# Performance work log

Measured on AMD Instinct MI355X. Metric: run time of the kernel, lower is better.

The kernel has to match this reference:

```python
import jax, jax.numpy as jnp
import numpy as np

NX, NY = 256, 256            # img_size
NUM_DET, VIEW = 368, 180
SDD, SCD = 1000.0, 500.0
DCD = SDD - SCD
DET_INT = 2.0
PX = 1.0                     # pixel_size
SHIFT = 0.0                  # no quarter offset


def _geometry():
    # Faithful numpy port of FP.param_setting (equally_spaced mode)
    d_beta = np.pi * 360.0 / VIEW / 180.0
    beta = np.linspace(0.0, (VIEW - 1) * d_beta, VIEW)
    axis_x = np.linspace(-NX / 2, NX / 2, NX + 1) * PX          # [NX+1]
    axis_y = np.linspace(-NY / 2, NY / 2, NY + 1) * PX          # [NY+1]
    range_det_x = np.ones(NUM_DET) * DCD
    range_det_y = np.linspace(-(NUM_DET - 1) / 2, (NUM_DET - 1) / 2, NUM_DET) * DET_INT + SHIFT
    src = np.array([-SCD, 0.0])
    cb, sb = np.cos(beta), np.sin(beta)
    src_point = np.stack([src[0] * cb + src[1] * sb, -src[0] * sb + src[1] * cb])  # [2, V]
    det_x_rot = cb[None, :] * range_det_x[:, None] + sb[None, :] * range_det_y[:, None]   # [D, V]
    det_y_rot = -sb[None, :] * range_det_x[:, None] + cb[None, :] * range_det_y[:, None]  # [D, V]
    ax = (axis_x[:, None] - src_point[0][None, :])[None, :, :] / (det_x_rot - src_point[0])[:, None, :]  # [D, NX+1, V]
    ay = (axis_y[:, None] - src_point[1][None, :])[None, :, :] / (det_y_rot - src_point[1])[:, None, :]  # [D, NY+1, V]
    a_min = np.maximum(np.minimum(ax[:, 0, :], ax[:, -1, :]), np.minimum(ay[:, 0, :], ay[:, -1, :]))
    a_min[a_min < 0] = 0.0
    a_max = np.minimum(np.maximum(ax[:, 0, :], ax[:, -1, :]), np.maximum(ay[:, 0, :], ay[:, -1, :]))
    a_max[a_max > 1] = 1.0
    axy = np.concatenate([ax, ay], axis=1)                       # [D, NX+NY+2, V]
    axy[(axy > a_max[:, None, :]) | (axy < a_min[:, None, :])] = np.nan
    axy = np.sort(axy, axis=1)                                   # NaNs sort to the end (matches torch)
    diff_axy = np.diff(axy, n=1, axis=1)                         # [D, S, V], S = NX+NY+1
    a_mid = axy[:, :-1, :] + diff_axy / 2
    diff_axy = np.nan_to_num(diff_axy, nan=0.0)
    a_mid = np.nan_to_num(a_mid, nan=0.0)
    s2d = np.sqrt((det_x_rot - src_point[0]) ** 2 + (det_y_rot - src_point[1]) ** 2)  # [D, V]
    weighting = diff_axy.transpose(0, 2, 1)[None, None] * s2d[None, None, :, :, None]  # [1,1,D,V,S]
    x_pos = a_mid * (det_x_rot[:, None, :] - src_point[0]) + src_point[0]
    x_pos = x_pos.transpose(0, 2, 1) / (PX * (NX - 1) / 2)       # [D, V, S]
    y_pos = a_mid * (det_y_rot[:, None, :] - src_point[1]) + src_point[1]
    y_pos = y_pos.transpose(0, 2, 1) / (PX * (NY - 1) / 2)
    grid_pos = np.stack([x_pos, y_pos], axis=-1)                 # [D, V, S, 2]
    return grid_pos.astype(np.float32), weighting.astype(np.float32)


def _bilinear_sample(img, gx, gy):
    # torch.nn.functional.grid_sample: bilinear, padding_mode='zeros', align_corners=False
    # img: [B,C,H,W]; gx indexes W, gy indexes H; gx/gy: [D,V,S]
    B, C, H, W = img.shape
    ix = ((gx + 1.0) * W - 1.0) * 0.5
    iy = ((gy + 1.0) * H - 1.0) * 0.5
    ix0 = jnp.floor(ix)
    iy0 = jnp.floor(iy)
    wx1 = ix - ix0
    wy1 = iy - iy0
    out = jnp.zeros((B, C) + gx.shape, dtype=img.dtype)
    for dx in (0, 1):
        for dy in (0, 1):
            xi = ix0 + dx
            yi = iy0 + dy
            w = (wx1 if dx else 1.0 - wx1) * (wy1 if dy else 1.0 - wy1)
            valid = (xi >= 0) & (xi < W) & (yi >= 0) & (yi < H)
            xi_c = jnp.clip(xi, 0, W - 1).astype(jnp.int32)
            yi_c = jnp.clip(yi, 0, H - 1).astype(jnp.int32)
            out = out + img[:, :, yi_c, xi_c] * (w * valid)[None, None]
    return out  # [B,C,D,V,S]


def setup_inputs() -> dict:
    key = jax.random.key(0)
    img = jax.random.normal(key, (1, 1, NX, NY), dtype=jnp.float32)
    gp, wt = _geometry()
    return {"img": img, "grid_pos": jnp.asarray(gp), "weighting": jnp.asarray(wt)}


def reference(img, grid_pos, weighting):
    # All views vectorized at once (torch version loops over views)
    interp = _bilinear_sample(img, grid_pos[..., 0], grid_pos[..., 1])  # [B,C,D,V,S]
    sino = jnp.sum(weighting * interp, axis=-1)                         # [B,C,D,V]
    return jnp.where(jnp.isnan(sino), jnp.zeros((), sino.dtype), sino)
```

## Files before the change

kernel.cpp:

```cpp
#include <hip/hip_runtime.h>
#include <hip/hip_fp16.h>
#include <math.h>


constexpr int IMG_N  = 256;
constexpr int NDET   = 368;
constexpr int NVIEW  = 180;
constexpr int NSAMP  = 2 * IMG_N + 1;
constexpr int DV     = NDET * NVIEW;
constexpr int NITER  = (NSAMP + 63) / 64;

struct __align__(8) Corner { __half2 ab; __half2 cd; };

constexpr size_t PACK_BYTES = (size_t)IMG_N * IMG_N * sizeof(Corner);
constexpr size_t RT_OFF     = PACK_BYTES;
constexpr size_t RT_BYTES   = (size_t)DV * 3 * sizeof(float4);
constexpr size_t KR_OFF     = RT_OFF + RT_BYTES;
constexpr size_t KR_BYTES   = (size_t)DV * sizeof(int2);
constexpr size_t WS_NEEDED  = KR_OFF + KR_BYTES;

__device__ __forceinline__ double valAP(double A, double s, double inv, int k) {
    return (A + s * (double)k) * inv;
}

__global__ __launch_bounds__(256) void pack_kernel(
    const float* __restrict__ img, Corner* __restrict__ P)
{
    const int idx = blockIdx.x * 256 + threadIdx.x;
    const int y  = idx >> 8;
    const int x  = idx & 255;
    const int x1 = min(x + 1, IMG_N - 1);
    const int y1 = min(y + 1, IMG_N - 1);
    Corner c;
    c.ab = __floats2half2_rn(img[y * IMG_N + x],  img[y * IMG_N + x1]);
    c.cd = __floats2half2_rn(img[y1 * IMG_N + x], img[y1 * IMG_N + x1]);
    P[idx] = c;
}

__global__ __launch_bounds__(256) void geom_kernel(
    float4* __restrict__ rt, int2* __restrict__ kr)
{
    const int idx = blockIdx.x * 256 + threadIdx.x;
    if (idx >= DV) return;
    const int d = idx / NVIEW;
    const int v = idx - d * NVIEW;

    const double d_beta = ((M_PI * 360.0) / (double)NVIEW) / 180.0;
    const double stop   = (double)(NVIEW - 1) * d_beta;
    const double step   = stop / (double)(NVIEW - 1);
    const double beta   = (v == NVIEW - 1) ? stop : (double)v * step;
    const double cb = cos(beta), sb = sin(beta);

    const double sx  = -500.0 * cb;
    const double sy  =  500.0 * sb;
    const double rdy = ((double)d - 183.5) * 2.0;
    const double dx  = cb * 500.0 + sb * rdy;
    const double dy  = (-sb) * 500.0 + cb * rdy;
    const double ddx = dx - sx, ddy = dy - sy;

    double Ax, sxn;
    const double invx = 1.0 / ddx;
    if (invx >= 0.0) { Ax = -128.0 - sx; sxn = 1.0; }
    else             { Ax =  128.0 - sx; sxn = -1.0; }
    double Ay, syn;
    const double invy = 1.0 / ddy;
    if (invy >= 0.0) { Ay = -128.0 - sy; syn = 1.0; }
    else             { Ay =  128.0 - sy; syn = -1.0; }

    const double vx0 = valAP(Ax, sxn, invx, 0), vxN = valAP(Ax, sxn, invx, IMG_N);
    const double vy0 = valAP(Ay, syn, invy, 0), vyN = valAP(Ay, syn, invy, IMG_N);
    double a_min = fmax(vx0, vy0); if (a_min < 0.0) a_min = 0.0;
    double a_max = fmin(vxN, vyN); if (a_max > 1.0) a_max = 1.0;

    const double absdx = fabs(ddx), absdy = fabs(ddy);

    int klox, khix, kloy, khiy;
    {
        double kd = (a_min - vx0) * absdx;
        kd = fmin(fmax(kd, -1.0), 258.0);
        int k = (int)kd; k = max(0, min(k, 256));
        while (k > 0    && valAP(Ax, sxn, invx, k - 1) >= a_min) --k;
        while (k <= 256 && valAP(Ax, sxn, invx, k) < a_min)      ++k;
        klox = k;
        kd = (a_max - vx0) * absdx;
        kd = fmin(fmax(kd, -1.0), 258.0);
        k = (int)kd; k = max(0, min(k, 256));
        while (k > 0    && valAP(Ax, sxn, invx, k - 1) > a_max)  --k;
        while (k <= 256 && valAP(Ax, sxn, invx, k) <= a_max)     ++k;
        khix = k - 1;
        if (klox > khix) { klox = 0; khix = -1; }
    }
    {
        double kd = (a_min - vy0) * absdy;
        kd = fmin(fmax(kd, -1.0), 258.0);
        int k = (int)kd; k = max(0, min(k, 256));
        while (k > 0    && valAP(Ay, syn, invy, k - 1) >= a_min) --k;
        while (k <= 256 && valAP(Ay, syn, invy, k) < a_min)      ++k;
        kloy = k;
        kd = (a_max - vy0) * absdy;
        kd = fmin(fmax(kd, -1.0), 258.0);
        k = (int)kd; k = max(0, min(k, 256));
        while (k > 0    && valAP(Ay, syn, invy, k - 1) > a_max)  --k;
        while (k <= 256 && valAP(Ay, syn, invy, k) <= a_max)     ++k;
        khiy = k - 1;
        if (kloy > khiy) { kloy = 0; khiy = -1; }
    }

    const int nx = khix - klox + 1;
    const int ny = khiy - kloy + 1;
    const double s2d = sqrt(ddx * ddx + ddy * ddy);

    const double sxd = sxn * invx, syd = syn * invy;
    const double bxd = (Ax + sxn * (double)klox) * invx;
    const double byd = (Ay + syn * (double)kloy) * invy;
    const double ssum = sxd + syd;
    const double c0 = (byd - bxd) / ssum;
    const double c1 = syd / ssum;

    float4* o = rt + (size_t)idx * 3;
    o[0] = make_float4((float)bxd, (float)sxd, (float)byd, (float)syd);
    o[1] = make_float4((float)c0, (float)c1, (float)s2d, 0.0f);
    o[2] = make_float4((float)(ddx * (128.0 / 127.5)),
                       (float)(sx  * (128.0 / 127.5) + 127.5),
                       (float)(ddy * (128.0 / 127.5)),
                       (float)(sy  * (128.0 / 127.5) + 127.5));
    kr[idx] = make_int2(nx, ny);
}

__device__ __forceinline__ float mergedq(int q, float bx, float sx, float by,
                                         float sy, float c0, float c1,
                                         int nx, int ny)
{
    const int t   = q + 1;
    const int mlo = max(0, t - ny);
    const int mhi = min(nx, t);
    int m = (int)fmaf((float)q, c1, c0);
    m = max(mlo, min(m, mhi));
    while (m > mlo) {
        const int mm = m - 1;
        const bool Pmm = (t - 1 - mm < 0) || (mm >= nx) ||
            (fmaf((float)(t - 1 - mm), sy, by) <= fmaf((float)mm, sx, bx));
        if (!Pmm) break;
        m = mm;
    }
    while (m < mhi) {
        const bool Pm = (t - 1 - m < 0) || (m >= nx) ||
            (fmaf((float)(t - 1 - m), sy, by) <= fmaf((float)m, sx, bx));
        if (Pm) break;
        ++m;
    }
    const float xl = (m > 0)     ? fmaf((float)(m - 1),     sx, bx) : -3e38f;
    const float yl = (t - m > 0) ? fmaf((float)(t - 1 - m), sy, by) : -3e38f;
    return fmaxf(xl, yl);
}

__global__ __launch_bounds__(256) void fp_siddon(
    const Corner* __restrict__ P,
    const float4* __restrict__ rt,
    const int2*   __restrict__ kr,
    float*        __restrict__ out)
{
    const int wave = threadIdx.x >> 6;
    const int lane = threadIdx.x & 63;
    const int dv   = __builtin_amdgcn_readfirstlane(blockIdx.x * 4 + wave);

    const float4 A = rt[(size_t)dv * 3 + 0];
    const float4 B = rt[(size_t)dv * 3 + 1];
    const float4 C = rt[(size_t)dv * 3 + 2];
    const int2 nn = kr[dv];
    const int nx = nn.x, ny = nn.y;
    const int M = nx + ny;
    const int npairs = M - 1;

    float acc = 0.0f;

    for (int base = 0; base < npairs; base += 64) {
        const int p = base + lane;
        const bool act = (p < npairs);
        const int q = act ? p + 1 : 1;

        const float cur = mergedq(q, A.x, A.y, A.z, A.w, B.x, B.y, nx, ny);
        float prev = __shfl_up(cur, 1, 64);
        if (lane == 0)
            prev = mergedq(base, A.x, A.y, A.z, A.w, B.x, B.y, nx, ny);

        const float diff = cur - prev;
        const float mid  = fmaf(diff, 0.5f, prev);
        const float ixp  = fmaf(mid, C.x, C.y);
        const float iyp  = fmaf(mid, C.z, C.w);
        const float wf   = act ? diff * B.z : 0.0f;

        const float fx0 = floorf(ixp), fy0 = floorf(iyp);
        const float wx1 = ixp - fx0,  wy1 = iyp - fy0;
        const int x0 = (int)fx0, y0 = (int)fy0;
        const int xc = min(max(x0, 0), IMG_N - 1);
        const int yb = min(max(y0, 0), IMG_N - 1);

        const Corner pc = P[yb * IMG_N + xc];
        const float2 r0 = __half22float2(pc.ab);
        const float2 r1 = __half22float2(pc.cd);

        const bool loX = (x0 == -1), loY = (y0 == -1);
        const float a  = r0.x;
        const float b2 = loX ? r0.x : r0.y;
        const float d2 = loX ? r1.x : r1.y;
        const float c3 = loY ? a  : r1.x;
        const float d3 = loY ? b2 : d2;
        const float x0v = (((unsigned)x0)       < 256u) ? 1.0f : 0.0f;
        const float x1v = (((unsigned)(x0 + 1)) < 256u) ? 1.0f : 0.0f;
        const float my0 = (((unsigned)y0)       < 256u) ? 1.0f : 0.0f;
        const float my1 = (((unsigned)(y0 + 1)) < 256u) ? 1.0f : 0.0f;
        const float wx0 = 1.0f - wx1;
        const float wy0 = (1.0f - wy1) * my0;
        const float wy1m = wy1 * my1;
        const float interp = (a * x0v * wx0 + b2 * x1v * wx1) * wy0
                           + (c3 * x0v * wx0 + d3 * x1v * wx1) * wy1m;

        acc = fmaf(wf, interp, acc);
    }

    #pragma unroll
    for (int off = 32; off > 0; off >>= 1)
        acc += __shfl_down(acc, off, 64);
    if (lane == 0)
        out[dv] = isnan(acc) ? 0.0f : acc;
}

__global__ __launch_bounds__(256) void fp_kernel_nopack(
    const float*  __restrict__ img,
    const float2* __restrict__ grid,
    const float*  __restrict__ wt,
    float*        __restrict__ out)
{
    const int wave = threadIdx.x >> 6;
    const int lane = threadIdx.x & 63;
    const int dv   = blockIdx.x * 4 + wave;
    const long base = (long)dv * NSAMP;

    float2 g[NITER];
    float  w[NITER];
    #pragma unroll
    for (int k = 0; k < NITER; ++k) {
        const int s = lane + k * 64;
        if (s < NSAMP) { g[k] = grid[base + s]; w[k] = wt[base + s]; }
        else           { g[k] = make_float2(0.0f, 0.0f); w[k] = 0.0f; }
    }
    float acc = 0.0f;
    #pragma unroll
    for (int k = 0; k < NITER; ++k) {
        const float ix = ((g[k].x + 1.0f) * 256.0f - 1.0f) * 0.5f;
        const float iy = ((g[k].y + 1.0f) * 256.0f - 1.0f) * 0.5f;
        const float fx0 = floorf(ix), fy0 = floorf(iy);
        const float wx1 = ix - fx0,  wy1 = iy - fy0;
        const int x0 = (int)fx0, y0 = (int)fy0;
        const int xc  = min(max(x0, 0), IMG_N - 2);
        const int yc0 = min(max(y0, 0), IMG_N - 1);
        const int yc1 = min(max(y0 + 1, 0), IMG_N - 1);
        const float2 p0 = *(const float2*)(img + yc0 * IMG_N + xc);
        const float2 p1 = *(const float2*)(img + yc1 * IMG_N + xc);
        const bool x0v = ((unsigned)x0) < 256u;
        const bool x1v = ((unsigned)(x0 + 1)) < 256u;
        const bool hiX = (x0 == IMG_N - 1);
        const bool loX = (x0 == -1);
        const float v00 = x0v ? (hiX ? p0.y : p0.x) : 0.0f;
        const float v01 = x1v ? (loX ? p0.x : p0.y) : 0.0f;
        const float v10 = x0v ? (hiX ? p1.y : p1.x) : 0.0f;
        const float v11 = x1v ? (loX ? p1.x : p1.y) : 0.0f;
        const float my0 = (((unsigned)y0) < 256u) ? 1.0f : 0.0f;
        const float my1 = (((unsigned)(y0 + 1)) < 256u) ? 1.0f : 0.0f;
        const float wx0 = 1.0f - wx1;
        const float wy0 = (1.0f - wy1) * my0;
        const float wy1m = wy1 * my1;
        acc += w[k] * ((v00 * wx0 + v01 * wx1) * wy0
                     + (v10 * wx0 + v11 * wx1) * wy1m);
    }
    #pragma unroll
    for (int off = 32; off > 0; off >>= 1)
        acc += __shfl_down(acc, off, 64);
    if (lane == 0) out[dv] = isnan(acc) ? 0.0f : acc;
}

extern "C" void kernel_launch(void* const* d_in, const int* in_sizes, int n_in,
                              void* d_out, int out_size, void* d_ws, size_t ws_size,
                              hipStream_t stream) {
    const float*  img  = (const float*)d_in[0];
    const float2* grid = (const float2*)d_in[1];
    const float*  wt   = (const float*)d_in[2];
    float*        out  = (float*)d_out;

    if (ws_size >= WS_NEEDED) {
        Corner* P  = (Corner*)d_ws;
        float4* rt = (float4*)((char*)d_ws + RT_OFF);
        int2*   kr = (int2*)  ((char*)d_ws + KR_OFF);
        pack_kernel<<<IMG_N * IMG_N / 256, 256, 0, stream>>>(img, P);
        geom_kernel<<<(DV + 255) / 256, 256, 0, stream>>>(rt, kr);
        fp_siddon<<<DV / 4, 256, 0, stream>>>(P, rt, kr, out);
    } else {
        fp_kernel_nopack<<<DV / 4, 256, 0, stream>>>(img, grid, wt, out);
    }
}
```

Baseline: 413.3 us.

## Stage fp16 image in LDS and gather bilinear corners from shared memory

Adds a path that converts the image to fp16 and has each 1024-thread block copy the whole 256x256 image into LDS, using a padded row stride. The block then processes 64 detector-view rays, four per wave, and reads the four bilinear corners from LDS instead of doing a packed-corner global gather per sample. The aim is to replace scattered L1/L2 traffic with cheaper LDS accesses. In exchange, every block reloads about 128 KB of image, only one block fits per CU so occupancy is capped, and the random LDS reads can hit bank conflicts. The path is chosen at runtime only when the device reports enough LDS per CU.

```diff
diff --git a/kernel.cpp b/kernel.cpp
--- a/kernel.cpp
+++ b/kernel.cpp
@@ -10,10 +10,13 @@
 constexpr int DV     = NDET * NVIEW;
 constexpr int NITER  = (NSAMP + 63) / 64;
 
+constexpr int LDS_STRIDE = 258;
+constexpr size_t LDS_BYTES = (size_t)IMG_N * LDS_STRIDE * 2;
+
 struct __align__(8) Corner { __half2 ab; __half2 cd; };
 
-constexpr size_t PACK_BYTES = (size_t)IMG_N * IMG_N * sizeof(Corner);
-constexpr size_t RT_OFF     = PACK_BYTES;
+constexpr size_t REG0_BYTES = (size_t)IMG_N * IMG_N * sizeof(Corner);
+constexpr size_t RT_OFF     = REG0_BYTES;
 constexpr size_t RT_BYTES   = (size_t)DV * 3 * sizeof(float4);
 constexpr size_t KR_OFF     = RT_OFF + RT_BYTES;
 constexpr size_t KR_BYTES   = (size_t)DV * sizeof(int2);
@@ -21,6 +24,13 @@
 
 __device__ __forceinline__ double valAP(double A, double s, double inv, int k) {
     return (A + s * (double)k) * inv;
+}
+
+__global__ __launch_bounds__(256) void pack16_kernel(
+    const float* __restrict__ img, __half* __restrict__ img16)
+{
+    const int i = blockIdx.x * 256 + threadIdx.x;
+    img16[i] = __float2half(img[i]);
 }
 
 __global__ __launch_bounds__(256) void pack_kernel(
@@ -154,6 +164,95 @@
     return fmaxf(xl, yl);
 }
 
+__global__ __launch_bounds__(1024) void fp_siddon_lds(
+    const __half* __restrict__ img16,
+    const float4* __restrict__ rt,
+    const int2*   __restrict__ kr,
+    float*        __restrict__ out)
+{
+    extern __shared__ __half simg[];
+    const int tid = threadIdx.x;
+
+    {
+        const unsigned* src = (const unsigned*)img16;
+        #pragma unroll
+        for (int i = 0; i < 32; ++i) {
+            const int u = i * 1024 + tid;
+            const unsigned val = src[u];
+            const int p = u * 2;
+            const int y = p >> 8;
+            const int x = p & 255;
+            *reinterpret_cast<unsigned*>(&simg[y * LDS_STRIDE + x]) = val;
+        }
+    }
+    __syncthreads();
+
+    const int wave = tid >> 6;
+    const int lane = tid & 63;
+
+    for (int r = 0; r < 4; ++r) {
+        const int dv = __builtin_amdgcn_readfirstlane(blockIdx.x * 64 + wave * 4 + r);
+
+        const float4 A = rt[(size_t)dv * 3 + 0];
+        const float4 B = rt[(size_t)dv * 3 + 1];
+        const float4 C = rt[(size_t)dv * 3 + 2];
+        const int2 nn = kr[dv];
+        const int nx = nn.x, ny = nn.y;
+        const int npairs = nx + ny - 1;
+
+        float acc = 0.0f;
+
+        for (int base = 0; base < npairs; base += 64) {
+            const int p = base + lane;
+            const bool act = (p < npairs);
+            const int q = act ? p + 1 : 1;
+
+            const float cur = mergedq(q, A.x, A.y, A.z, A.w, B.x, B.y, nx, ny);
+            float prev = __shfl_up(cur, 1, 64);
+            if (lane == 0)
+                prev = mergedq(base, A.x, A.y, A.z, A.w, B.x, B.y, nx, ny);
+
+            const float diff = cur - prev;
+            const float mid  = fmaf(diff, 0.5f, prev);
+            const float ixp  = fmaf(mid, C.x, C.y);
+            const float iyp  = fmaf(mid, C.z, C.w);
+            const float wf   = act ? diff * B.z : 0.0f;
+
+            const float fx0 = floorf(ixp), fy0 = floorf(iyp);
+            const float wx1 = ixp - fx0,  wy1 = iyp - fy0;
+            const int x0 = (int)fx0, y0 = (int)fy0;
+
+            const int xc0 = min(max(x0, 0), IMG_N - 1);
+            const int xc1 = min(max(x0 + 1, 0), IMG_N - 1);
+            const int hb0 = min(max(y0, 0), IMG_N - 1) * LDS_STRIDE;
+            const int hb1 = min(max(y0 + 1, 0), IMG_N - 1) * LDS_STRIDE;
+
+            const float v00 = __half2float(simg[hb0 + xc0]);
+            const float v01 = __half2float(simg[hb0 + xc1]);
+            const float v10 = __half2float(simg[hb1 + xc0]);
+            const float v11 = __half2float(simg[hb1 + xc1]);
+
+            const float x0v = (((unsigned)x0)       < 256u) ? 1.0f : 0.0f;
+            const float x1v = (((unsigned)(x0 + 1)) < 256u) ? 1.0f : 0.0f;
+            const float my0 = (((unsigned)y0)       < 256u) ? 1.0f : 0.0f;
+            const float my1 = (((unsigned)(y0 + 1)) < 256u) ? 1.0f : 0.0f;
+            const float wx0 = 1.0f - wx1;
+            const float wy0 = (1.0f - wy1) * my0;
+            const float wy1m = wy1 * my1;
+            const float interp = (v00 * x0v * wx0 + v01 * x1v * wx1) * wy0
+                               + (v10 * x0v * wx0 + v11 * x1v * wx1) * wy1m;
+
+            acc = fmaf(wf, interp, acc);
+        }
+
+        #pragma unroll
+        for (int off = 32; off > 0; off >>= 1)
+            acc += __shfl_down(acc, off, 64);
+        if (lane == 0)
+            out[dv] = isnan(acc) ? 0.0f : acc;
+    }
+}
+
 __global__ __launch_bounds__(256) void fp_siddon(
     const Corner* __restrict__ P,
     const float4* __restrict__ rt,
@@ -169,37 +268,30 @@
     const float4 C = rt[(size_t)dv * 3 + 2];
     const int2 nn = kr[dv];
     const int nx = nn.x, ny = nn.y;
-    const int M = nx + ny;
-    const int npairs = M - 1;
+    const int npairs = nx + ny - 1;
 
     float acc = 0.0f;
-
     for (int base = 0; base < npairs; base += 64) {
         const int p = base + lane;
         const bool act = (p < npairs);
         const int q = act ? p + 1 : 1;
-
         const float cur = mergedq(q, A.x, A.y, A.z, A.w, B.x, B.y, nx, ny);
         float prev = __shfl_up(cur, 1, 64);
         if (lane == 0)
             prev = mergedq(base, A.x, A.y, A.z, A.w, B.x, B.y, nx, ny);
-
         const float diff = cur - prev;
         const float mid  = fmaf(diff, 0.5f, prev);
         const float ixp  = fmaf(mid, C.x, C.y);
         const float iyp  = fmaf(mid, C.z, C.w);
         const float wf   = act ? diff * B.z : 0.0f;
-
         const float fx0 = floorf(ixp), fy0 = floorf(iyp);
         const float wx1 = ixp - fx0,  wy1 = iyp - fy0;
         const int x0 = (int)fx0, y0 = (int)fy0;
         const int xc = min(max(x0, 0), IMG_N - 1);
         const int yb = min(max(y0, 0), IMG_N - 1);
-
         const Corner pc = P[yb * IMG_N + xc];
         const float2 r0 = __half22float2(pc.ab);
         const float2 r1 = __half22float2(pc.cd);
-
         const bool loX = (x0 == -1), loY = (y0 == -1);
         const float a  = r0.x;
         const float b2 = loX ? r0.x : r0.y;
@@ -215,10 +307,8 @@
         const float wy1m = wy1 * my1;
         const float interp = (a * x0v * wx0 + b2 * x1v * wx1) * wy0
                            + (c3 * x0v * wx0 + d3 * x1v * wx1) * wy1m;
-
         acc = fmaf(wf, interp, acc);
     }
-
     #pragma unroll
     for (int off = 32; off > 0; off >>= 1)
         acc += __shfl_down(acc, off, 64);
@@ -289,12 +379,27 @@
     float*        out  = (float*)d_out;
 
     if (ws_size >= WS_NEEDED) {
-        Corner* P  = (Corner*)d_ws;
         float4* rt = (float4*)((char*)d_ws + RT_OFF);
         int2*   kr = (int2*)  ((char*)d_ws + KR_OFF);
-        pack_kernel<<<IMG_N * IMG_N / 256, 256, 0, stream>>>(img, P);
-        geom_kernel<<<(DV + 255) / 256, 256, 0, stream>>>(rt, kr);
-        fp_siddon<<<DV / 4, 256, 0, stream>>>(P, rt, kr, out);
+
+        int dev = 0, smemCU = 0;
+        hipGetDevice(&dev);
+        hipDeviceGetAttribute(&smemCU,
+            hipDeviceAttributeMaxSharedMemoryPerMultiprocessor, dev);
+
+        if ((size_t)smemCU >= LDS_BYTES) {
+            __half* img16 = (__half*)d_ws;
+            (void)hipFuncSetAttribute((const void*)fp_siddon_lds,
+                hipFuncAttributeMaxDynamicSharedMemorySize, (int)LDS_BYTES);
+            pack16_kernel<<<IMG_N * IMG_N / 256, 256, 0, stream>>>(img, img16);
+            geom_kernel<<<(DV + 255) / 256, 256, 0, stream>>>(rt, kr);
+            fp_siddon_lds<<<DV / 64, 1024, LDS_BYTES, stream>>>(img16, rt, kr, out);
+        } else {
+            Corner* P = (Corner*)d_ws;
+            pack_kernel<<<IMG_N * IMG_N / 256, 256, 0, stream>>>(img, P);
+            geom_kernel<<<(DV + 255) / 256, 256, 0, stream>>>(rt, kr);
+            fp_siddon<<<DV / 4, 256, 0, stream>>>(P, rt, kr, out);
+        }
     } else {
         fp_kernel_nopack<<<DV / 4, 256, 0, stream>>>(img, grid, wt, out);
     }
```

New measurement: 459.1 us. +11.1%, slower.
